# Performance work log

Hardware: AMD Instinct MI355X
Metric: run time of the kernel (lower is better)

## Reference

```python
import jax, jax.numpy as jnp
import numpy as np

N = 8192      # nodes
E = 16384     # edges
G = 512       # graphs
IN = 235      # node feature dim (input_dim)
H = 64        # hidden_dim
ED = 52       # edge feature dim


def setup_inputs() -> dict:
    key = jax.random.key(0)
    ks = jax.random.split(key, 24)
    s = lambda fan_in: 1.0 / np.sqrt(fan_in)
    inp = {}
    inp["x"] = jax.random.normal(ks[0], (N, IN), dtype=jnp.float32)
    inp["edge_index"] = jax.random.randint(ks[1], (2, E), 0, N)
    inp["edge_attr"] = jax.random.uniform(ks[2], (E, ED), dtype=jnp.float32)
    inp["batch"] = jnp.sort(jax.random.randint(ks[3], (N,), 0, G))
    # EdgeModel (nn of nnconv1): Linear(52,128) -> Linear(128, 235*64)
    inp["W1"] = jax.random.normal(ks[4], (128, ED), dtype=jnp.float32) * s(ED)
    inp["b1"] = jnp.zeros((128,), jnp.float32)
    inp["W2"] = jax.random.normal(ks[5], (IN * H, 128), dtype=jnp.float32) * s(128)
    inp["b2"] = jnp.zeros((IN * H,), jnp.float32)
    # NNConv root weight and bias
    inp["root"] = jax.random.normal(ks[6], (IN, H), dtype=jnp.float32) * s(IN)
    inp["conv_b"] = jnp.zeros((H,), jnp.float32)
    # MLP head
    inp["fw1"] = jax.random.normal(ks[7], (128, H), dtype=jnp.float32) * s(H)
    inp["fb1"] = jnp.zeros((128,), jnp.float32)
    inp["fw2"] = jax.random.normal(ks[8], (256, 128), dtype=jnp.float32) * s(128)
    inp["fb2"] = jnp.zeros((256,), jnp.float32)
    inp["fw3"] = jax.random.normal(ks[9], (128, 256), dtype=jnp.float32) * s(256)
    inp["fb3"] = jnp.zeros((128,), jnp.float32)
    inp["fw4"] = jax.random.normal(ks[10], (1, 128), dtype=jnp.float32) * s(128)
    inp["fb4"] = jnp.zeros((1,), jnp.float32)
    return inp


def reference(x, edge_index, edge_attr, batch, W1, b1, W2, b2, root, conv_b,
              fw1, fb1, fw2, fb2, fw3, fb3, fw4, fb4):
    src, dst = edge_index[0], edge_index[1]
    # edge MLP -> per-edge weight matrices [E, IN, H]
    h = edge_attr @ W1.T + b1
    w = (h @ W2.T + b2).reshape(E, IN, H)
    # gather source node feats, per-edge matmul, scatter-add to destinations
    msg = jnp.einsum('ei,eih->eh', x[src], w)          # [E, H]
    agg = jax.ops.segment_sum(msg, dst, num_segments=N)  # [N, H]
    out = jax.nn.relu(agg + x @ root + conv_b)           # NNConv + ReLU
    # global mean pool per graph
    summ = jax.ops.segment_sum(out, batch, num_segments=G)
    cnt = jax.ops.segment_sum(jnp.ones((N, 1), out.dtype), batch, num_segments=G)
    pooled = summ / jnp.maximum(cnt, 1.0)                # [G, H]
    # dense MLP head
    y = jax.nn.relu(pooled @ fw1.T + fb1)
    y = jax.nn.relu(y @ fw2.T + fb2)
    y = jax.nn.relu(y @ fw3.T + fb3)
    return y @ fw4.T + fb4                               # [G, 1]
```

## Files before the change

### kernel.cpp

```cpp
#include <hip/hip_runtime.h>
#include <hip/hip_bf16.h>
#include <stdint.h>

#define N_NODES 8192
#define N_EDGES 16384
#define N_GRAPHS 512
#define IN_DIM 235
#define H_DIM 64
#define ED_DIM 52
#define HID1 128
#define KP 256
#define NB 3328
#define NBE 3456

typedef __bf16 bf16x8 __attribute__((ext_vector_type(8)));
typedef float f32x4 __attribute__((ext_vector_type(4)));

static __device__ inline unsigned short f2bf(float f) {
    union { float f; unsigned u; } v; v.f = f;
    unsigned r = v.u + 0x7FFFu + ((v.u >> 16) & 1u);
    return (unsigned short)(r >> 16);
}
static __device__ inline float bf2f(unsigned short s) {
    union { unsigned u; float f; } v; v.u = ((unsigned)s) << 16;
    return v.f;
}

__global__ __launch_bounds__(256) void k_build_bt(const float* __restrict__ W1,
                                                  const float* __restrict__ W2,
                                                  unsigned short* __restrict__ Bt) {
    __shared__ float w1s[13 * HID1];
    __shared__ float w2s[64 * 132];
    const int i = blockIdx.x;
    const int by = blockIdx.y;
    const int t = threadIdx.x;
    const int dbase = by * 13;
    for (int j = t; j < 13 * HID1; j += 256) {
        const int dd = j >> 7, k = j & 127;
        w1s[j] = W1[k * ED_DIM + dbase + dd];
    }
    const float* w2src = W2 + (size_t)i * 64 * HID1;
    for (int j = t; j < 64 * HID1; j += 256) w2s[(j >> 7) * 132 + (j & 127)] = w2src[j];
    __syncthreads();
    const int pend = by * 832 + 832;
    for (int p = by * 832 + t; p < pend; p += 256) {
        const int dd = (p >> 6) - dbase, h = p & 63;
        const float4* w1v = (const float4*)&w1s[dd * HID1];
        const float4* w2v = (const float4*)&w2s[h * 132];
        float acc = 0.f;
        #pragma unroll
        for (int k4 = 0; k4 < HID1 / 4; ++k4) {
            const float4 a = w1v[k4], b = w2v[k4];
            acc += a.x * b.x + a.y * b.y + a.z * b.z + a.w * b.w;
        }
        Bt[(size_t)p * KP + i] = f2bf(acc);
    }
}

__global__ __launch_bounds__(256) void k_build_bc(const float* __restrict__ W2,
                                                  const float* __restrict__ b1,
                                                  const float* __restrict__ b2,
                                                  float* __restrict__ bc) {
    const int j = blockIdx.x * 256 + threadIdx.x;
    if (j >= IN_DIM * H_DIM) return;
    float acc = b2[j];
    const float* w = W2 + (size_t)j * HID1;
    #pragma unroll 8
    for (int k = 0; k < HID1; ++k) acc += w[k] * b1[k];
    bc[j] = acc;
}

__global__ __launch_bounds__(256) void k_build_ext(const float* __restrict__ root,
                                                   const float* __restrict__ bc,
                                                   unsigned short* __restrict__ Bt) {
    const int j = blockIdx.x;
    const int i = threadIdx.x;
    if (i >= IN_DIM) return;
    const float v = (j < 64) ? root[i * H_DIM + j] : bc[i * H_DIM + (j - 64)];
    Bt[(size_t)(NB + j) * KP + i] = f2bf(v);
}

__global__ __launch_bounds__(256) void k_build_a(const float* __restrict__ x,
                                                 unsigned short* __restrict__ A) {
    const int j = blockIdx.x * 256 + threadIdx.x;
    const int n = j >> 8, i = j & 255;
    A[j] = (i < IN_DIM) ? f2bf(x[n * IN_DIM + i]) : (unsigned short)0;
}

__global__ __launch_bounds__(256) void k_gemm(const unsigned short* __restrict__ A,
                                              const unsigned short* __restrict__ Bt,
                                              unsigned short* __restrict__ P,
                                              float* __restrict__ agg,
                                              float* __restrict__ xb2,
                                              const float* __restrict__ conv_b) {
    __shared__ unsigned short As[128 * 32];
    __shared__ unsigned short Bs[128 * 32];
    const int t = threadIdx.x;
    const int m0 = blockIdx.y * 128, n0 = blockIdx.x * 128;
    const int wid = t >> 6, lane = t & 63;
    const int wm = wid >> 1, wn = wid & 1;
    const int q = lane >> 4, r16 = lane & 15;

    f32x4 acc[4][4] = {};

    for (int k0 = 0; k0 < KP; k0 += 32) {
        __syncthreads();
        #pragma unroll
        for (int r = 0; r < 2; ++r) {
            const int idx = r * 256 + t;
            const int row = idx >> 2;
            const int lgrp = (((idx & 3) ^ ((row >> 1) & 3))) * 8;
            const unsigned short* ga = &A[(size_t)(m0 + row) * KP + k0 + lgrp];
            const unsigned short* gb = &Bt[(size_t)(n0 + row) * KP + k0 + lgrp];
            char* la = (char*)As + r * 4096 + wid * 1024;
            char* lb = (char*)Bs + r * 4096 + wid * 1024;
            __builtin_amdgcn_global_load_lds(
                (const __attribute__((address_space(1))) unsigned int*)ga,
                (__attribute__((address_space(3))) unsigned int*)la, 16, 0, 0);
            __builtin_amdgcn_global_load_lds(
                (const __attribute__((address_space(1))) unsigned int*)gb,
                (__attribute__((address_space(3))) unsigned int*)lb, 16, 0, 0);
        }
        __syncthreads();
        bf16x8 af[4], bfr[4];
        const int pcq = (q ^ ((r16 >> 1) & 3)) * 8;
        #pragma unroll
        for (int mi = 0; mi < 4; ++mi)
            af[mi] = *(const bf16x8*)(&As[(wm * 64 + mi * 16 + r16) * 32 + pcq]);
        #pragma unroll
        for (int ni = 0; ni < 4; ++ni)
            bfr[ni] = *(const bf16x8*)(&Bs[(wn * 64 + ni * 16 + r16) * 32 + pcq]);
        #pragma unroll
        for (int mi = 0; mi < 4; ++mi)
            #pragma unroll
            for (int ni = 0; ni < 4; ++ni)
                acc[mi][ni] = __builtin_amdgcn_mfma_f32_16x16x32_bf16(
                    bfr[ni], af[mi], acc[mi][ni], 0, 0, 0);
    }

    if (n0 < NB) {
        #pragma unroll
        for (int mi = 0; mi < 4; ++mi)
            #pragma unroll
            for (int ni = 0; ni < 4; ++ni) {
                const int row = m0 + wm * 64 + mi * 16 + r16;
                const int col = n0 + wn * 64 + ni * 16 + q * 4;
                union { unsigned short us[4]; uint2 u2; } pk;
                #pragma unroll
                for (int rr = 0; rr < 4; ++rr) pk.us[rr] = f2bf(acc[mi][ni][rr]);
                *(uint2*)(&P[(size_t)row * NB + col]) = pk.u2;
            }
    } else {
        #pragma unroll
        for (int mi = 0; mi < 4; ++mi)
            #pragma unroll
            for (int ni = 0; ni < 4; ++ni) {
                const int row = m0 + wm * 64 + mi * 16 + r16;
                const int cl = ni * 16 + q * 4;
                if (wn == 0) {
                    const float4 cb = *(const float4*)&conv_b[cl];
                    float4 v;
                    v.x = acc[mi][ni][0] + cb.x; v.y = acc[mi][ni][1] + cb.y;
                    v.z = acc[mi][ni][2] + cb.z; v.w = acc[mi][ni][3] + cb.w;
                    *(float4*)(&agg[row * H_DIM + cl]) = v;
                } else {
                    float4 v;
                    v.x = acc[mi][ni][0]; v.y = acc[mi][ni][1];
                    v.z = acc[mi][ni][2]; v.w = acc[mi][ni][3];
                    *(float4*)(&xb2[row * H_DIM + cl]) = v;
                }
            }
    }
}

__global__ __launch_bounds__(256) void k_edge(const int* __restrict__ ei,
                                              const float* __restrict__ ea,
                                              const unsigned short* __restrict__ P,
                                              const float* __restrict__ xb2,
                                              float* __restrict__ agg) {
    const int e = (blockIdx.x * 256 + threadIdx.x) >> 6;
    const int h = threadIdx.x & 63;
    if (e >= N_EDGES) return;
    const int s = ei[e], dst = ei[N_EDGES + e];
    const unsigned short* Pr = P + (size_t)s * NB;
    const float* ear = ea + (size_t)e * ED_DIM;
    float acc = xb2[s * H_DIM + h];
    #pragma unroll 4
    for (int d = 0; d < ED_DIM; ++d)
        acc += ear[d] * bf2f(Pr[d * H_DIM + h]);
    atomicAdd(&agg[dst * H_DIM + h], acc);
}

__global__ __launch_bounds__(256) void k_pool(const float* __restrict__ agg,
                                              const int* __restrict__ batch,
                                              float* __restrict__ psum,
                                              float* __restrict__ pcnt) {
    const int n = (blockIdx.x * 256 + threadIdx.x) >> 6;
    const int h = threadIdx.x & 63;
    if (n >= N_NODES) return;
    const float v = fmaxf(agg[n * H_DIM + h], 0.f);
    const int g = batch[n];
    atomicAdd(&psum[g * H_DIM + h], v);
    if (h == 0) atomicAdd(&pcnt[g], 1.0f);
}

__global__ __launch_bounds__(256) void k_head(const float* __restrict__ psum,
                                              const float* __restrict__ pcnt,
                                              const float* __restrict__ fw1, const float* __restrict__ fb1,
                                              const float* __restrict__ fw2, const float* __restrict__ fb2,
                                              const float* __restrict__ fw3, const float* __restrict__ fb3,
                                              const float* __restrict__ fw4, const float* __restrict__ fb4,
                                              float* __restrict__ out) {
    __shared__ float sp[64], s1[128], s2[256], s3[128];
    const int g = blockIdx.x, t = threadIdx.x;
    if (t < 64) sp[t] = psum[g * 64 + t] / fmaxf(pcnt[g], 1.0f);
    __syncthreads();
    if (t < 128) {
        float a = fb1[t];
        const float* w = fw1 + t * 64;
        #pragma unroll 8
        for (int k = 0; k < 64; ++k) a += sp[k] * w[k];
        s1[t] = fmaxf(a, 0.f);
    }
    __syncthreads();
    {
        float a = fb2[t];
        const float* w = fw2 + t * 128;
        #pragma unroll 8
        for (int k = 0; k < 128; ++k) a += s1[k] * w[k];
        s2[t] = fmaxf(a, 0.f);
    }
    __syncthreads();
    if (t < 128) {
        float a = fb3[t];
        const float* w = fw3 + t * 256;
        #pragma unroll 8
        for (int k = 0; k < 256; ++k) a += s2[k] * w[k];
        s3[t] = fmaxf(a, 0.f);
    }
    __syncthreads();
    if (t < 64) {
        float p = s3[t] * fw4[t] + s3[t + 64] * fw4[t + 64];
        #pragma unroll
        for (int off = 32; off > 0; off >>= 1) p += __shfl_down(p, off);
        if (t == 0) out[g] = p + fb4[0];
    }
}

extern "C" void kernel_launch(void* const* d_in, const int* in_sizes, int n_in,
                              void* d_out, int out_size, void* d_ws, size_t ws_size,
                              hipStream_t stream) {
    const float* x      = (const float*)d_in[0];
    const int*   ei     = (const int*)d_in[1];
    const float* ea     = (const float*)d_in[2];
    const int*   batch  = (const int*)d_in[3];
    const float* W1     = (const float*)d_in[4];
    const float* b1     = (const float*)d_in[5];
    const float* W2     = (const float*)d_in[6];
    const float* b2     = (const float*)d_in[7];
    const float* root   = (const float*)d_in[8];
    const float* conv_b = (const float*)d_in[9];
    const float* fw1 = (const float*)d_in[10]; const float* fb1 = (const float*)d_in[11];
    const float* fw2 = (const float*)d_in[12]; const float* fb2 = (const float*)d_in[13];
    const float* fw3 = (const float*)d_in[14]; const float* fb3 = (const float*)d_in[15];
    const float* fw4 = (const float*)d_in[16]; const float* fb4 = (const float*)d_in[17];
    float* out = (float*)d_out;

    char* ws = (char*)d_ws;
    unsigned short* A   = (unsigned short*)(ws);
    unsigned short* Bt  = (unsigned short*)(ws + 4194304);
    unsigned short* P   = (unsigned short*)(ws + 5963776);
    float* agg  = (float*)(ws + 60489728);
    float* xb2  = (float*)(ws + 62586880);
    float* bc   = (float*)(ws + 64684032);
    float* psum = (float*)(ws + 64744192);
    float* pcnt = (float*)(ws + 64875264);

    hipMemsetAsync(Bt, 0, (size_t)NBE * KP * sizeof(unsigned short), stream);
    hipMemsetAsync(psum, 0, (size_t)(N_GRAPHS * H_DIM + N_GRAPHS) * sizeof(float), stream);

    k_build_bc<<<dim3((IN_DIM * H_DIM + 255) / 256), dim3(256), 0, stream>>>(W2, b1, b2, bc);
    k_build_bt<<<dim3(IN_DIM, 4), dim3(256), 0, stream>>>(W1, W2, Bt);
    k_build_ext<<<dim3(128), dim3(256), 0, stream>>>(root, bc, Bt);
    k_build_a<<<dim3(N_NODES), dim3(256), 0, stream>>>(x, A);
    k_gemm<<<dim3(NBE / 128, N_NODES / 128), dim3(256), 0, stream>>>(A, Bt, P, agg, xb2, conv_b);
    k_edge<<<dim3(N_EDGES / 4), dim3(256), 0, stream>>>(ei, ea, P, xb2, agg);
    k_pool<<<dim3(N_NODES / 4), dim3(256), 0, stream>>>(agg, batch, psum, pcnt);
    k_head<<<dim3(N_GRAPHS), dim3(256), 0, stream>>>(psum, pcnt, fw1, fb1, fw2, fb2, fw3, fb3, fw4, fb4, out);
}
```

Measured before the change: 225.9 us.

## Double-buffer GEMM LDS tiles and batch edge-kernel loads for more parallelism

The GEMM k-loop now uses two LDS buffers, so the next K slice is fetched asynchronously while MFMAs run on the current one, with a single barrier per iteration. The edge kernel preloads all 52 edge-attribute floats with float4 loads and all 52 P values into registers before the dot product, exposing memory-level parallelism instead of a serialized load-FMA chain. This doubles LDS use per block and raises register pressure in the edge kernel, which may lower occupancy.

```diff
diff --git a/kernel.cpp b/kernel.cpp
--- a/kernel.cpp
+++ b/kernel.cpp
@@ -93,8 +93,8 @@
                                               float* __restrict__ agg,
                                               float* __restrict__ xb2,
                                               const float* __restrict__ conv_b) {
-    __shared__ unsigned short As[128 * 32];
-    __shared__ unsigned short Bs[128 * 32];
+    __shared__ unsigned short As[2 * 128 * 32];
+    __shared__ unsigned short Bs[2 * 128 * 32];
     const int t = threadIdx.x;
     const int m0 = blockIdx.y * 128, n0 = blockIdx.x * 128;
     const int wid = t >> 6, lane = t & 63;
@@ -103,17 +103,16 @@
 
     f32x4 acc[4][4] = {};
 
-    for (int k0 = 0; k0 < KP; k0 += 32) {
-        __syncthreads();
+    auto stage = [&](int k0, int buf) {
         #pragma unroll
         for (int r = 0; r < 2; ++r) {
             const int idx = r * 256 + t;
             const int row = idx >> 2;
-            const int lgrp = (((idx & 3) ^ ((row >> 1) & 3))) * 8;
+            const int lgrp = ((idx & 3) ^ ((row >> 1) & 3)) * 8;
             const unsigned short* ga = &A[(size_t)(m0 + row) * KP + k0 + lgrp];
             const unsigned short* gb = &Bt[(size_t)(n0 + row) * KP + k0 + lgrp];
-            char* la = (char*)As + r * 4096 + wid * 1024;
-            char* lb = (char*)Bs + r * 4096 + wid * 1024;
+            char* la = (char*)As + buf * 8192 + r * 4096 + wid * 1024;
+            char* lb = (char*)Bs + buf * 8192 + r * 4096 + wid * 1024;
             __builtin_amdgcn_global_load_lds(
                 (const __attribute__((address_space(1))) unsigned int*)ga,
                 (__attribute__((address_space(3))) unsigned int*)la, 16, 0, 0);
@@ -121,15 +120,22 @@
                 (const __attribute__((address_space(1))) unsigned int*)gb,
                 (__attribute__((address_space(3))) unsigned int*)lb, 16, 0, 0);
         }
+    };
+
+    stage(0, 0);
+    const int pcq = (q ^ ((r16 >> 1) & 3)) * 8;
+    #pragma unroll
+    for (int it = 0; it < 8; ++it) {
         __syncthreads();
+        if (it < 7) stage((it + 1) * 32, (it + 1) & 1);
+        const int bo = (it & 1) * 4096;
         bf16x8 af[4], bfr[4];
-        const int pcq = (q ^ ((r16 >> 1) & 3)) * 8;
         #pragma unroll
         for (int mi = 0; mi < 4; ++mi)
-            af[mi] = *(const bf16x8*)(&As[(wm * 64 + mi * 16 + r16) * 32 + pcq]);
+            af[mi] = *(const bf16x8*)(&As[bo + (wm * 64 + mi * 16 + r16) * 32 + pcq]);
         #pragma unroll
         for (int ni = 0; ni < 4; ++ni)
-            bfr[ni] = *(const bf16x8*)(&Bs[(wn * 64 + ni * 16 + r16) * 32 + pcq]);
+            bfr[ni] = *(const bf16x8*)(&Bs[bo + (wn * 64 + ni * 16 + r16) * 32 + pcq]);
         #pragma unroll
         for (int mi = 0; mi < 4; ++mi)
             #pragma unroll
@@ -182,12 +188,21 @@
     const int h = threadIdx.x & 63;
     if (e >= N_EDGES) return;
     const int s = ei[e], dst = ei[N_EDGES + e];
-    const unsigned short* Pr = P + (size_t)s * NB;
+    const unsigned short* Pr = P + (size_t)s * NB + h;
     const float* ear = ea + (size_t)e * ED_DIM;
+
+    float eav[ED_DIM];
+    #pragma unroll
+    for (int d4 = 0; d4 < ED_DIM / 4; ++d4)
+        *(float4*)&eav[d4 * 4] = *(const float4*)&ear[d4 * 4];
+
+    unsigned short pv[ED_DIM];
+    #pragma unroll
+    for (int d = 0; d < ED_DIM; ++d) pv[d] = Pr[d * H_DIM];
+
     float acc = xb2[s * H_DIM + h];
-    #pragma unroll 4
-    for (int d = 0; d < ED_DIM; ++d)
-        acc += ear[d] * bf2f(Pr[d * H_DIM + h]);
+    #pragma unroll
+    for (int d = 0; d < ED_DIM; ++d) acc += eav[d] * bf2f(pv[d]);
     atomicAdd(&agg[dst * H_DIM + h], acc);
 }
 
```

Result: no change. 228.8 us (+1.3%).
